# Optimization experiments

Hardware: AMD Instinct MI355X
Metric: run time of the kernel (lower is better)

Reference implementation:

```python
import jax, jax.numpy as jnp
import numpy as np
import math

N = 50000          # n_nodes
E = 1600000        # n_edges (avg degree 32)
D = 256            # input_size
H = 8              # n_heads
HS = D // H        # head_size = 32


def setup_inputs() -> dict:
    key = jax.random.key(0)
    k1, k2, k3, k4, k5 = jax.random.split(key, 5)
    X = jax.random.normal(k1, (N, D), dtype=jnp.float32)
    # xavier_uniform for [D, HS] weight: bound = sqrt(6 / (fan_in + fan_out))
    bound = math.sqrt(6.0 / (D + HS))
    Wq = jax.random.uniform(k2, (D, HS), jnp.float32, -bound, bound)
    Wk = jax.random.uniform(k3, (D, HS), jnp.float32, -bound, bound)
    Wv = jax.random.uniform(k4, (D, HS), jnp.float32, -bound, bound)
    edge_index = jax.random.randint(k5, (2, E), 0, N, dtype=jnp.int32)
    return {"X": X, "Wq": Wq, "Wk": Wk, "Wv": Wv, "edge_index": edge_index}


def reference(X, Wq, Wk, Wv, edge_index):
    # Projections: [N, HS]
    Q = X @ Wq
    K = X @ Wk
    V = X @ Wv
    r = edge_index[0]  # row (query) node per edge
    c = edge_index[1]  # col (key/value) node per edge
    dk = jnp.asarray(math.sqrt(HS), dtype=X.dtype)
    # Edge-level attention logits: [E]
    scores = jnp.sum(Q[r] * K[c], axis=-1) / dk
    # Sparse row-wise (dim=1) softmax over existing edges only.
    row_max = jax.ops.segment_max(scores, r, num_segments=N)   # -inf for empty rows
    ex = jnp.exp(scores - row_max[r])                          # [E]
    denom = jax.ops.segment_sum(ex, r, num_segments=N)         # [N]
    # Weighted V aggregation: [N, HS]
    num = jax.ops.segment_sum(ex[:, None] * V[c], r, num_segments=N)
    # Rows with no incident edges produce zeros (matches sparse softmax + to_dense @ V).
    safe = jnp.maximum(denom, jnp.asarray(1e-30, X.dtype))[:, None]
    return jnp.where(denom[:, None] > 0, num / safe, jnp.zeros_like(num))
```

## Files before the change

kernel.cpp:

```cpp
#include <hip/hip_runtime.h>

#define N_NODES 50000
#define N_EDGES 1600000
#define D_IN    256
#define HS      32

#define NB      1250
#define ROWS_PB 40
#define CAP     1600
#define EPB     4096

#define MTILE   64
#define PROJ_B  ((N_NODES + MTILE - 1) / MTILE)
#define BIN_B   ((N_EDGES + EPB - 1) / EPB)

typedef __bf16 bf16x8 __attribute__((ext_vector_type(8)));
typedef float  floatx4 __attribute__((ext_vector_type(4)));

static __device__ __forceinline__ unsigned short f2bf(float f) {
    unsigned u = __float_as_uint(f);
    return (unsigned short)((u + 0x7FFFu + ((u >> 16) & 1u)) >> 16);
}

__global__ __launch_bounds__(256) void wfrag_kernel(
    const float* __restrict__ Wq, const float* __restrict__ Wk,
    const float* __restrict__ Wv, unsigned short* __restrict__ wfrag,
    int* __restrict__ fill, int* __restrict__ rowptr)
{
    if (blockIdx.x == 0) {
        for (int b = threadIdx.x; b < NB; b += 256) fill[b] = 0;
        if (threadIdx.x == 0) rowptr[N_NODES] = N_EDGES;
    }
    const int i = blockIdx.x * blockDim.x + threadIdx.x;
    if (i >= 8 * 6 * 64 * 8) return;
    const int j    = i & 7;
    const int lane = (i >> 3) & 63;
    const int st   = i >> 9;
    const int t    = st % 6;
    const int s    = st / 6;
    const int k    = s * 32 + (lane >> 4) * 8 + j;
    const int col  = t * 16 + (lane & 15);
    float v;
    if      (col < 32) v = Wq[k * HS + col];
    else if (col < 64) v = Wk[k * HS + (col - 32)];
    else               v = Wv[k * HS + (col - 64)];
    wfrag[i] = f2bf(v);
}

__global__ __launch_bounds__(256) void proj_bin_kernel(
    const float* __restrict__ X, const unsigned short* __restrict__ wfrag,
    float* __restrict__ Q, unsigned int* __restrict__ KVp,
    const int* __restrict__ er, const int* __restrict__ ec,
    int* __restrict__ fill, unsigned int* __restrict__ pairs)
{
    __shared__ int lcnt[NB];

    const int t = threadIdx.x;
    const int mod = blockIdx.x % 3;

    if (mod != 2) {
        const int pb   = (blockIdx.x / 3) * 2 + mod;
        const int lane = t & 63;
        const int w    = t >> 6;
        const int quad = lane >> 4;
        const int m16  = lane & 15;
        const int row0 = pb * MTILE;

        const int arow = w * 16 + m16;
        const int grc  = min(row0 + arow, N_NODES - 1);
        const float* xrow = X + (size_t)grc * D_IN;

        floatx4 acc[6];
#pragma unroll
        for (int nt = 0; nt < 6; nt++) acc[nt] = (floatx4)0.f;

#pragma unroll
        for (int s = 0; s < 8; s++) {
            const float4 a0 = *(const float4*)(xrow + s * 32 + quad * 8);
            const float4 a1 = *(const float4*)(xrow + s * 32 + quad * 8 + 4);
            union { bf16x8 v; unsigned short u[8]; } af;
            af.u[0] = f2bf(a0.x); af.u[1] = f2bf(a0.y);
            af.u[2] = f2bf(a0.z); af.u[3] = f2bf(a0.w);
            af.u[4] = f2bf(a1.x); af.u[5] = f2bf(a1.y);
            af.u[6] = f2bf(a1.z); af.u[7] = f2bf(a1.w);
            bf16x8 bfr[6];
#pragma unroll
            for (int nt = 0; nt < 6; nt++)
                bfr[nt] = *(const bf16x8*)(wfrag + (((s * 6 + nt) * 64 + lane) * 8));
#pragma unroll
            for (int nt = 0; nt < 6; nt++)
                acc[nt] = __builtin_amdgcn_mfma_f32_16x16x32_bf16(af.v, bfr[nt], acc[nt], 0, 0, 0);
        }

#pragma unroll
        for (int i = 0; i < 4; i++) {
            const int gr = row0 + w * 16 + quad * 4 + i;
            if (gr < N_NODES) {
#pragma unroll
                for (int nt = 0; nt < 2; nt++)
                    Q[gr * HS + nt * 16 + m16] = acc[nt][i];
#pragma unroll
                for (int p = 0; p < 2; p++) {
                    const int j = p * 16 + m16;
                    const unsigned kb = f2bf(acc[2 + p][i]);
                    const unsigned vb = f2bf(acc[4 + p][i]);
                    KVp[gr * HS + j] = (kb << 16) | vb;
                }
            }
        }
    } else {
        const int bb = blockIdx.x / 3;
        const int e0 = bb * EPB;
        const int e1 = min(e0 + EPB, N_EDGES);

        for (int b = t; b < NB; b += 256) lcnt[b] = 0;
        __syncthreads();

        int rl[16], cl[16];
#pragma unroll
        for (int i = 0; i < 16; i++) {
            const int e = e0 + t + i * 256;
            if (e < e1) {
                rl[i] = er[e];
                cl[i] = ec[e];
                atomicAdd(&lcnt[rl[i] / ROWS_PB], 1);
            }
        }
        __syncthreads();

        for (int b = t; b < NB; b += 256) {
            const int c = lcnt[b];
            lcnt[b] = (c > 0) ? atomicAdd(&fill[b], c) : 0;
        }
        __syncthreads();

#pragma unroll
        for (int i = 0; i < 16; i++) {
            const int e = e0 + t + i * 256;
            if (e < e1) {
                const int r = rl[i];
                const int b = r / ROWS_PB;
                const int slot = atomicAdd(&lcnt[b], 1);
                pairs[(size_t)b * CAP + slot] =
                    ((unsigned)(r - b * ROWS_PB) << 16) | (unsigned)cl[i];
            }
        }
    }
}

__global__ __launch_bounds__(256) void place_kernel(
    const unsigned int* __restrict__ pairs, const int* __restrict__ fill,
    int* __restrict__ rowptr, int* __restrict__ col_sorted)
{
    __shared__ int hist[4][ROWS_PB];
    __shared__ int s[64];
    __shared__ int red[256];
    __shared__ int stage[CAP];

    const int b = blockIdx.x;
    const int t = threadIdx.x;
    const int w = t >> 6;
    const int n = fill[b];
    const unsigned int* pb = pairs + (size_t)b * CAP;

    int partial = 0;
    for (int i = t; i < b; i += 256) partial += fill[i];
    red[t] = partial;
    if (t < 4 * ROWS_PB) ((int*)hist)[t] = 0;
    __syncthreads();
#pragma unroll
    for (int ofs = 128; ofs > 0; ofs >>= 1) {
        if (t < ofs) red[t] += red[t + ofs];
        __syncthreads();
    }
    const int base = red[0];

    unsigned pl[(CAP + 255) / 256];
#pragma unroll
    for (int k = 0; k < (CAP + 255) / 256; k++) {
        const int i = t + k * 256;
        if (i < n) {
            pl[k] = pb[i];
            atomicAdd(&hist[w][pl[k] >> 16], 1);
        }
    }
    __syncthreads();

    if (t < 64)
        s[t] = (t < ROWS_PB) ? (hist[0][t] + hist[1][t] + hist[2][t] + hist[3][t]) : 0;
    __syncthreads();
#pragma unroll
    for (int ofs = 1; ofs < 64; ofs <<= 1) {
        int u = 0;
        if (t < 64 && t >= ofs) u = s[t - ofs];
        __syncthreads();
        if (t < 64) s[t] += u;
        __syncthreads();
    }
    if (t < ROWS_PB) {
        const int h0 = hist[0][t], h1 = hist[1][t], h2 = hist[2][t], h3 = hist[3][t];
        const int excl = s[t] - (h0 + h1 + h2 + h3);
        rowptr[b * ROWS_PB + t] = base + excl;
        int run = excl;
        hist[0][t] = run; run += h0;
        hist[1][t] = run; run += h1;
        hist[2][t] = run; run += h2;
        hist[3][t] = run;
    }
    __syncthreads();

#pragma unroll
    for (int k = 0; k < (CAP + 255) / 256; k++) {
        const int i = t + k * 256;
        if (i < n) {
            const unsigned p = pl[k];
            const int pos = atomicAdd(&hist[w][p >> 16], 1);
            stage[pos] = (int)(p & 0xFFFFu);
        }
    }
    __syncthreads();

    for (int i = t; i < n; i += 256)
        col_sorted[base + i] = stage[i];
}

__global__ __launch_bounds__(256) void aggregate_kernel(
    const int* __restrict__ rowptr, const int* __restrict__ col,
    const float* __restrict__ Q, const unsigned int* __restrict__ KVp,
    float* __restrict__ out)
{
    const int lane = threadIdx.x & 63;
    const int r    = (blockIdx.x * blockDim.x + threadIdx.x) >> 6;
    if (r >= N_NODES) return;
    const int comp = lane & 7;
    const int slot = lane >> 3;

    const float4 q4 = *(const float4*)(Q + r * HS + comp * 4);
    const int start = rowptr[r];
    const int end   = rowptr[r + 1];
    const int last  = end - 1;
    const float scale = 0.17677669529663687f;

    float accD = 0.f;
    float n0 = 0.f, n1 = 0.f, n2 = 0.f, n3 = 0.f;

    for (int e0 = start; e0 < end; e0 += 32) {
        int   cc[4];
        uint4 kv[4];
#pragma unroll
        for (int b = 0; b < 4; b++)
            if (e0 + 8 * b < end)
                cc[b] = col[min(e0 + 8 * b + slot, last)];
#pragma unroll
        for (int b = 0; b < 4; b++)
            if (e0 + 8 * b < end)
                kv[b] = *(const uint4*)(KVp + (size_t)cc[b] * HS + comp * 4);
#pragma unroll
        for (int b = 0; b < 4; b++) {
            if (e0 + 8 * b < end) {
                float p = q4.x * __uint_as_float(kv[b].x & 0xFFFF0000u)
                        + q4.y * __uint_as_float(kv[b].y & 0xFFFF0000u)
                        + q4.z * __uint_as_float(kv[b].z & 0xFFFF0000u)
                        + q4.w * __uint_as_float(kv[b].w & 0xFFFF0000u);
#pragma unroll
                for (int ofs = 1; ofs < 8; ofs <<= 1)
                    p += __shfl_xor(p, ofs, 64);
                const float ex = (e0 + 8 * b + slot < end) ? __expf(p * scale) : 0.f;
                accD += ex;
                n0 += ex * __uint_as_float(kv[b].x << 16);
                n1 += ex * __uint_as_float(kv[b].y << 16);
                n2 += ex * __uint_as_float(kv[b].z << 16);
                n3 += ex * __uint_as_float(kv[b].w << 16);
            }
        }
    }

#pragma unroll
    for (int ofs = 8; ofs < 64; ofs <<= 1) {
        accD += __shfl_xor(accD, ofs, 64);
        n0 += __shfl_xor(n0, ofs, 64);
        n1 += __shfl_xor(n1, ofs, 64);
        n2 += __shfl_xor(n2, ofs, 64);
        n3 += __shfl_xor(n3, ofs, 64);
    }

    if (slot == 0) {
        const float inv = (accD > 0.f) ? 1.f / accD : 0.f;
        float4 o;
        o.x = n0 * inv; o.y = n1 * inv; o.z = n2 * inv; o.w = n3 * inv;
        *(float4*)(out + r * HS + comp * 4) = o;
    }
}

extern "C" void kernel_launch(void* const* d_in, const int* in_sizes, int n_in,
                              void* d_out, int out_size, void* d_ws, size_t ws_size,
                              hipStream_t stream)
{
    const float* X  = (const float*)d_in[0];
    const float* Wq = (const float*)d_in[1];
    const float* Wk = (const float*)d_in[2];
    const float* Wv = (const float*)d_in[3];
    const int*   ei = (const int*)d_in[4];
    const int* er = ei;
    const int* ec = ei + N_EDGES;

    float* out = (float*)d_out;

    float* Q          = (float*)d_ws;
    unsigned int* KVp = (unsigned int*)(Q + (size_t)N_NODES * HS);
    int* fill         = (int*)(KVp + (size_t)N_NODES * HS);
    int* rowptr       = fill + NB;
    unsigned short* wfrag = (unsigned short*)(rowptr + (N_NODES + 1));
    unsigned int* pairs   = (unsigned int*)(wfrag + 8 * 6 * 64 * 8);
    int* col_sorted   = (int*)(pairs + (size_t)NB * CAP);

    wfrag_kernel<<<(8 * 6 * 64 * 8 + 255) / 256, 256, 0, stream>>>(
        Wq, Wk, Wv, wfrag, fill, rowptr);

    proj_bin_kernel<<<PROJ_B + BIN_B, 256, 0, stream>>>(
        X, wfrag, Q, KVp, er, ec, fill, pairs);

    place_kernel<<<NB, 256, 0, stream>>>(pairs, fill, rowptr, col_sorted);

    aggregate_kernel<<<(N_NODES * 64 + 255) / 256, 256, 0, stream>>>(
        rowptr, col_sorted, Q, KVp, out);
}
```

Baseline: 158.9 us.

## Fuse bucket sort with attention aggregation, drop global CSR materialization

The per-bucket counting sort and the row aggregation are merged into one kernel. Each block sorts its 40-row bucket in shared memory and then processes those rows directly, one wavefront per row, 10 rows per wave. This removes the global rowptr/col_sorted writes and reads, the cross-bucket prefix sum, and one kernel launch. The zeroing of fill moves to a hipMemsetAsync. In exchange, only 1250 blocks of 4 waves run the gather phase, so parallelism is lower and load imbalance between rows is serialized within each wave.

Result: no change. 160.3 us (+0.9%).

```diff
diff --git a/kernel.cpp b/kernel.cpp
--- a/kernel.cpp
+++ b/kernel.cpp
@@ -9,10 +9,11 @@
 #define ROWS_PB 40
 #define CAP     1600
 #define EPB     4096
+#define BIN_B   ((N_EDGES + EPB - 1) / EPB)
 
 #define MTILE   64
 #define PROJ_B  ((N_NODES + MTILE - 1) / MTILE)
-#define BIN_B   ((N_EDGES + EPB - 1) / EPB)
+#define GRID_F  (PROJ_B + BIN_B)
 
 typedef __bf16 bf16x8 __attribute__((ext_vector_type(8)));
 typedef float  floatx4 __attribute__((ext_vector_type(4)));
@@ -24,13 +25,8 @@
 
 __global__ __launch_bounds__(256) void wfrag_kernel(
     const float* __restrict__ Wq, const float* __restrict__ Wk,
-    const float* __restrict__ Wv, unsigned short* __restrict__ wfrag,
-    int* __restrict__ fill, int* __restrict__ rowptr)
+    const float* __restrict__ Wv, unsigned short* __restrict__ wfrag)
 {
-    if (blockIdx.x == 0) {
-        for (int b = threadIdx.x; b < NB; b += 256) fill[b] = 0;
-        if (threadIdx.x == 0) rowptr[N_NODES] = N_EDGES;
-    }
     const int i = blockIdx.x * blockDim.x + threadIdx.x;
     if (i >= 8 * 6 * 64 * 8) return;
     const int j    = i & 7;
@@ -59,7 +55,8 @@
     const int mod = blockIdx.x % 3;
 
     if (mod != 2) {
-        const int pb   = (blockIdx.x / 3) * 2 + mod;
+        const int pb = (blockIdx.x / 3) * 2 + mod;
+        if (pb >= PROJ_B) return;
         const int lane = t & 63;
         const int w    = t >> 6;
         const int quad = lane >> 4;
@@ -148,65 +145,58 @@
     }
 }
 
-__global__ __launch_bounds__(256) void place_kernel(
+__global__ __launch_bounds__(256) void bucket_agg_kernel(
     const unsigned int* __restrict__ pairs, const int* __restrict__ fill,
-    int* __restrict__ rowptr, int* __restrict__ col_sorted)
+    const float* __restrict__ Q, const unsigned int* __restrict__ KVp,
+    float* __restrict__ out)
 {
+    __shared__ unsigned srt[CAP];
     __shared__ int hist[4][ROWS_PB];
-    __shared__ int s[64];
-    __shared__ int red[256];
-    __shared__ int stage[CAP];
+    __shared__ int sc[64];
+    __shared__ int rowstart[ROWS_PB + 1];
 
     const int b = blockIdx.x;
     const int t = threadIdx.x;
     const int w = t >> 6;
     const int n = fill[b];
-    const unsigned int* pb = pairs + (size_t)b * CAP;
-
-    int partial = 0;
-    for (int i = t; i < b; i += 256) partial += fill[i];
-    red[t] = partial;
-    if (t < 4 * ROWS_PB) ((int*)hist)[t] = 0;
-    __syncthreads();
-#pragma unroll
-    for (int ofs = 128; ofs > 0; ofs >>= 1) {
-        if (t < ofs) red[t] += red[t + ofs];
-        __syncthreads();
-    }
-    const int base = red[0];
+    const unsigned int* pbk = pairs + (size_t)b * CAP;
+
+    for (int i = t; i < 4 * ROWS_PB; i += 256) ((int*)hist)[i] = 0;
+    __syncthreads();
 
     unsigned pl[(CAP + 255) / 256];
 #pragma unroll
     for (int k = 0; k < (CAP + 255) / 256; k++) {
         const int i = t + k * 256;
         if (i < n) {
-            pl[k] = pb[i];
+            pl[k] = pbk[i];
             atomicAdd(&hist[w][pl[k] >> 16], 1);
         }
     }
     __syncthreads();
 
     if (t < 64)
-        s[t] = (t < ROWS_PB) ? (hist[0][t] + hist[1][t] + hist[2][t] + hist[3][t]) : 0;
+        sc[t] = (t < ROWS_PB) ? (hist[0][t] + hist[1][t] + hist[2][t] + hist[3][t]) : 0;
     __syncthreads();
 #pragma unroll
     for (int ofs = 1; ofs < 64; ofs <<= 1) {
         int u = 0;
-        if (t < 64 && t >= ofs) u = s[t - ofs];
-        __syncthreads();
-        if (t < 64) s[t] += u;
+        if (t < 64 && t >= ofs) u = sc[t - ofs];
+        __syncthreads();
+        if (t < 64) sc[t] += u;
         __syncthreads();
     }
     if (t < ROWS_PB) {
         const int h0 = hist[0][t], h1 = hist[1][t], h2 = hist[2][t], h3 = hist[3][t];
-        const int excl = s[t] - (h0 + h1 + h2 + h3);
-        rowptr[b * ROWS_PB + t] = base + excl;
+        const int excl = sc[t] - (h0 + h1 + h2 + h3);
+        rowstart[t] = excl;
         int run = excl;
         hist[0][t] = run; run += h0;
         hist[1][t] = run; run += h1;
         hist[2][t] = run; run += h2;
         hist[3][t] = run;
     }
+    if (t == 0) rowstart[ROWS_PB] = n;
     __syncthreads();
 
 #pragma unroll
@@ -215,80 +205,74 @@
         if (i < n) {
             const unsigned p = pl[k];
             const int pos = atomicAdd(&hist[w][p >> 16], 1);
-            stage[pos] = (int)(p & 0xFFFFu);
-        }
-    }
-    __syncthreads();
-
-    for (int i = t; i < n; i += 256)
-        col_sorted[base + i] = stage[i];
-}
-
-__global__ __launch_bounds__(256) void aggregate_kernel(
-    const int* __restrict__ rowptr, const int* __restrict__ col,
-    const float* __restrict__ Q, const unsigned int* __restrict__ KVp,
-    float* __restrict__ out)
-{
-    const int lane = threadIdx.x & 63;
-    const int r    = (blockIdx.x * blockDim.x + threadIdx.x) >> 6;
-    if (r >= N_NODES) return;
+            srt[pos] = p & 0xFFFFu;
+        }
+    }
+    __syncthreads();
+
+    const int lane = t & 63;
     const int comp = lane & 7;
     const int slot = lane >> 3;
-
-    const float4 q4 = *(const float4*)(Q + r * HS + comp * 4);
-    const int start = rowptr[r];
-    const int end   = rowptr[r + 1];
-    const int last  = end - 1;
     const float scale = 0.17677669529663687f;
 
-    float accD = 0.f;
-    float n0 = 0.f, n1 = 0.f, n2 = 0.f, n3 = 0.f;
-
-    for (int e0 = start; e0 < end; e0 += 32) {
-        int   cc[4];
-        uint4 kv[4];
-#pragma unroll
-        for (int b = 0; b < 4; b++)
-            if (e0 + 8 * b < end)
-                cc[b] = col[min(e0 + 8 * b + slot, last)];
-#pragma unroll
-        for (int b = 0; b < 4; b++)
-            if (e0 + 8 * b < end)
-                kv[b] = *(const uint4*)(KVp + (size_t)cc[b] * HS + comp * 4);
-#pragma unroll
-        for (int b = 0; b < 4; b++) {
-            if (e0 + 8 * b < end) {
-                float p = q4.x * __uint_as_float(kv[b].x & 0xFFFF0000u)
-                        + q4.y * __uint_as_float(kv[b].y & 0xFFFF0000u)
-                        + q4.z * __uint_as_float(kv[b].z & 0xFFFF0000u)
-                        + q4.w * __uint_as_float(kv[b].w & 0xFFFF0000u);
-#pragma unroll
-                for (int ofs = 1; ofs < 8; ofs <<= 1)
-                    p += __shfl_xor(p, ofs, 64);
-                const float ex = (e0 + 8 * b + slot < end) ? __expf(p * scale) : 0.f;
-                accD += ex;
-                n0 += ex * __uint_as_float(kv[b].x << 16);
-                n1 += ex * __uint_as_float(kv[b].y << 16);
-                n2 += ex * __uint_as_float(kv[b].z << 16);
-                n3 += ex * __uint_as_float(kv[b].w << 16);
+#pragma unroll
+    for (int rr = 0; rr < ROWS_PB / 4; rr++) {
+        const int lr = w + rr * 4;
+        const int gr = b * ROWS_PB + lr;
+        const float4 q4 = *(const float4*)(Q + gr * HS + comp * 4);
+        const int start = rowstart[lr];
+        const int end   = rowstart[lr + 1];
+        const int last  = end - 1;
+
+        float accD = 0.f;
+        float n0 = 0.f, n1 = 0.f, n2 = 0.f, n3 = 0.f;
+
+        for (int e0 = start; e0 < end; e0 += 32) {
+            int   cc[4];
+            uint4 kv[4];
+#pragma unroll
+            for (int bb = 0; bb < 4; bb++)
+                if (e0 + 8 * bb < end)
+                    cc[bb] = (int)srt[min(e0 + 8 * bb + slot, last)];
+#pragma unroll
+            for (int bb = 0; bb < 4; bb++)
+                if (e0 + 8 * bb < end)
+                    kv[bb] = *(const uint4*)(KVp + (size_t)cc[bb] * HS + comp * 4);
+#pragma unroll
+            for (int bb = 0; bb < 4; bb++) {
+                if (e0 + 8 * bb < end) {
+                    float p = q4.x * __uint_as_float(kv[bb].x & 0xFFFF0000u)
+                            + q4.y * __uint_as_float(kv[bb].y & 0xFFFF0000u)
+                            + q4.z * __uint_as_float(kv[bb].z & 0xFFFF0000u)
+                            + q4.w * __uint_as_float(kv[bb].w & 0xFFFF0000u);
+#pragma unroll
+                    for (int ofs = 1; ofs < 8; ofs <<= 1)
+                        p += __shfl_xor(p, ofs, 64);
+                    const float ex = (e0 + 8 * bb + slot < end) ? __expf(p * scale) : 0.f;
+                    accD += ex;
+                    n0 += ex * __uint_as_float(kv[bb].x << 16);
+                    n1 += ex * __uint_as_float(kv[bb].y << 16);
+                    n2 += ex * __uint_as_float(kv[bb].z << 16);
+                    n3 += ex * __uint_as_float(kv[bb].w << 16);
+                }
             }
         }
-    }
-
-#pragma unroll
-    for (int ofs = 8; ofs < 64; ofs <<= 1) {
-        accD += __shfl_xor(accD, ofs, 64);
-        n0 += __shfl_xor(n0, ofs, 64);
-        n1 += __shfl_xor(n1, ofs, 64);
-        n2 += __shfl_xor(n2, ofs, 64);
-        n3 += __shfl_xor(n3, ofs, 64);
-    }
-
-    if (slot == 0) {
-        const float inv = (accD > 0.f) ? 1.f / accD : 0.f;
-        float4 o;
-        o.x = n0 * inv; o.y = n1 * inv; o.z = n2 * inv; o.w = n3 * inv;
-        *(float4*)(out + r * HS + comp * 4) = o;
+
+#pragma unroll
+        for (int ofs = 8; ofs < 64; ofs <<= 1) {
+            accD += __shfl_xor(accD, ofs, 64);
+            n0 += __shfl_xor(n0, ofs, 64);
+            n1 += __shfl_xor(n1, ofs, 64);
+            n2 += __shfl_xor(n2, ofs, 64);
+            n3 += __shfl_xor(n3, ofs, 64);
+        }
+
+        if (slot == 0) {
+            const float inv = (accD > 0.f) ? 1.f / accD : 0.f;
+            float4 o;
+            o.x = n0 * inv; o.y = n1 * inv; o.z = n2 * inv; o.w = n3 * inv;
+            *(float4*)(out + gr * HS + comp * 4) = o;
+        }
     }
 }
 
@@ -309,19 +293,16 @@
     float* Q          = (float*)d_ws;
     unsigned int* KVp = (unsigned int*)(Q + (size_t)N_NODES * HS);
     int* fill         = (int*)(KVp + (size_t)N_NODES * HS);
-    int* rowptr       = fill + NB;
-    unsigned short* wfrag = (unsigned short*)(rowptr + (N_NODES + 1));
+    unsigned short* wfrag = (unsigned short*)(fill + NB);
     unsigned int* pairs   = (unsigned int*)(wfrag + 8 * 6 * 64 * 8);
-    int* col_sorted   = (int*)(pairs + (size_t)NB * CAP);
+
+    hipMemsetAsync(fill, 0, NB * sizeof(int), stream);
 
     wfrag_kernel<<<(8 * 6 * 64 * 8 + 255) / 256, 256, 0, stream>>>(
-        Wq, Wk, Wv, wfrag, fill, rowptr);
-
-    proj_bin_kernel<<<PROJ_B + BIN_B, 256, 0, stream>>>(
+        Wq, Wk, Wv, wfrag);
+
+    proj_bin_kernel<<<GRID_F, 256, 0, stream>>>(
         X, wfrag, Q, KVp, er, ec, fill, pairs);
 
-    place_kernel<<<NB, 256, 0, stream>>>(pairs, fill, rowptr, col_sorted);
-
-    aggregate_kernel<<<(N_NODES * 64 + 255) / 256, 256, 0, stream>>>(
-        rowptr, col_sorted, Q, KVp, out);
-}
+    bucket_agg_kernel<<<NB, 256, 0, stream>>>(pairs, fill, Q, KVp, out);
+}
```
